# Kernel tuning notes

Measured on AMD Instinct MI355X. Metric: run time of the kernel, lower is better.

The kernel has to match this reference:

```python
import jax, jax.numpy as jnp
import numpy as np

H = 12  # num_heads (init kwarg)


def setup_inputs() -> dict:
    key = jax.random.key(0)
    ks = jax.random.split(key, 9)
    B, S, D, M = 2, 1025, 768, 4
    hw = S - 1
    x = jax.random.normal(ks[0], (B, S, D), dtype=jnp.float32)
    masks = jax.random.randint(ks[1], (B, M, hw), 0, 2, dtype=jnp.int32)
    init = lambda k: jax.random.normal(k, (D, D), dtype=jnp.float32) * 0.02
    return {
        'x': x, 'masks': masks,
        'Wq': init(ks[2]), 'bq': jnp.zeros((D,), jnp.float32),
        'Wk': init(ks[3]), 'bk': jnp.zeros((D,), jnp.float32),
        'Wv': init(ks[4]), 'bv': jnp.zeros((D,), jnp.float32),
    }


def reference(x, masks, Wq, bq, Wk, bk, Wv, bv):
    B, S, D = x.shape
    hd = D // H
    scale = 1.0 / jnp.sqrt(jnp.asarray(hd, x.dtype))

    def heads(t):  # (B,S,D) -> (B,H,S,hd)
        return t.reshape(B, S, H, hd).transpose(0, 2, 1, 3)

    q = heads(x @ Wq.T + bq)
    k = heads(x @ Wk.T + bk)
    v = heads(x @ Wv.T + bv)

    scores_ori = jnp.einsum('bhqd,bhkd->bhqk', q, k) * scale  # (B,H,S,S)
    attn = jax.nn.softmax(scores_ori, axis=-1)  # dropout is identity at eval
    h = jnp.einsum('bhqk,bhkd->bhqd', attn, v)
    h = h.transpose(0, 2, 1, 3).reshape(B, S, D)

    # ---- mask-expanded attention (torch.no_grad branch) ----
    Mk, hw = masks.shape[1], masks.shape[2]
    m = masks.astype(x.dtype)  # (B,M,hw)
    # pad: position 0 (CLS) gets 0, positions 1..hw get the mask
    new_masks = jnp.pad(m, ((0, 0), (0, 0), (1, S - 1 - hw)))  # (B,M,S)
    bias = -10000.0 * (1.0 - new_masks)  # additive mask bias
    new_scores = scores_ori[:, None] + bias[:, :, None, None, :]  # (B,M,H,S,S)
    new_attn = jax.nn.softmax(new_scores, axis=-1)
    new_h = jnp.einsum('bmhqk,bhkd->bmhqd', new_attn, v)  # v repeated per mask
    new_h = new_h.transpose(0, 1, 3, 2, 4).reshape(B * Mk, S, D)

    img_idx = jnp.repeat(jnp.arange(B), Mk)  # [0]*M + [1]*M + ...
    new_x = jnp.broadcast_to(x[:, None], (B, Mk, S, D)).reshape(B * Mk, S, D)
    return (h, new_h, img_idx, new_x)
```

## Files before the change

kernel.cpp:

```cpp
#include <hip/hip_runtime.h>

typedef float f32x4 __attribute__((ext_vector_type(4)));
typedef short s16x8 __attribute__((ext_vector_type(8)));

constexpr int B  = 2;
constexpr int S  = 1025;
constexpr int D  = 768;
constexpr int H  = 12;
constexpr int NM = 4;
constexpr int ROWS = B * S;
constexpr int BSD  = B * S * D;
constexpr int SP   = 1088;
constexpr int OUT_NEWH_OFF = BSD;
constexpr int OUT_IDX_OFF  = BSD + NM * BSD;
constexpr int OUT_NEWX_OFF = OUT_IDX_OFF + B * NM;

__device__ __forceinline__ unsigned short f2bf(float f) {
    unsigned u = __builtin_bit_cast(unsigned, f);
    u += 0x7FFF + ((u >> 16) & 1);
    return (unsigned short)(u >> 16);
}

__global__ __launch_bounds__(256, 2) void qkv_mfma_kernel(
    const float* __restrict__ x,
    const float* __restrict__ Wq, const float* __restrict__ bq,
    const float* __restrict__ Wk, const float* __restrict__ bk,
    const float* __restrict__ Wv, const float* __restrict__ bv,
    unsigned short* __restrict__ Qb, unsigned short* __restrict__ Kb,
    unsigned short* __restrict__ Vt)
{
    __shared__ unsigned short Xs[64 * 64];
    __shared__ unsigned short Wl[64 * 64];

    const int t = threadIdx.x;
    const int row0 = blockIdx.x * 64;
    const int yy = blockIdx.y;
    const int mt = yy / 12;
    const int col0 = (yy % 12) * 64;
    const float* W    = (mt == 0) ? Wq : (mt == 1) ? Wk : Wv;
    const float* bias = (mt == 0) ? bq : (mt == 1) ? bk : bv;

    const int w = t >> 6, l = t & 63, lq = l & 15, grp = l >> 4;

    f32x4 acc[4] = {};

    for (int k0 = 0; k0 < D; k0 += 64) {
        __syncthreads();
        #pragma unroll
        for (int st = 0; st < 2; ++st) {
            const int cid = t + st * 256;
            const int r = cid >> 3, c = cid & 7;
            {
                const int row = row0 + r;
                s16x8 v = {};
                if (row < ROWS) {
                    const float* p = x + (size_t)row * D + k0 + c * 8;
                    #pragma unroll
                    for (int i = 0; i < 8; i++) v[i] = (short)f2bf(p[i]);
                }
                *(s16x8*)&Xs[r * 64 + ((c ^ (r & 7)) * 8)] = v;
            }
            {
                const float* p = W + (size_t)(col0 + r) * D + k0 + c * 8;
                s16x8 v;
                #pragma unroll
                for (int i = 0; i < 8; i++) v[i] = (short)f2bf(p[i]);
                *(s16x8*)&Wl[r * 64 + ((c ^ (r & 7)) * 8)] = v;
            }
        }
        __syncthreads();

        s16x8 a[2];
        const int xr = w * 16 + lq;
        #pragma unroll
        for (int kh = 0; kh < 2; ++kh)
            a[kh] = *(const s16x8*)&Xs[xr * 64 + (((kh * 4 + grp) ^ (lq & 7)) * 8)];
        #pragma unroll
        for (int nt = 0; nt < 4; ++nt) {
            const int wr = nt * 16 + lq;
            #pragma unroll
            for (int kh = 0; kh < 2; ++kh) {
                s16x8 bfr = *(const s16x8*)&Wl[wr * 64 + (((kh * 4 + grp) ^ (lq & 7)) * 8)];
                acc[nt] = __builtin_amdgcn_mfma_f32_16x16x32_bf16(a[kh], bfr, acc[nt], 0, 0, 0);
            }
        }
    }

    #pragma unroll
    for (int nt = 0; nt < 4; ++nt) {
        const int col = col0 + nt * 16 + lq;
        const float bv_ = bias[col];
        #pragma unroll
        for (int r = 0; r < 4; ++r) {
            const int row = row0 + w * 16 + grp * 4 + r;
            if (row >= ROWS) continue;
            const unsigned short val = f2bf(acc[nt][r] + bv_);
            if (mt == 0)      Qb[(size_t)row * D + col] = val;
            else if (mt == 1) Kb[(size_t)row * D + col] = val;
            else {
                const int bb = (row >= S) ? 1 : 0;
                const int s  = row - bb * S;
                const int hh = col >> 6, dd = col & 63;
                Vt[((size_t)((bb * H + hh) * 64 + dd)) * SP + s] = val;
            }
        }
    }
}

__global__ void vt_pad_kernel(unsigned short* __restrict__ Vt)
{
    const int NPADC = SP - S;
    const int NPAD = B * H * 64 * NPADC;
    const int i = blockIdx.x * 256 + threadIdx.x;
    if (i < NPAD) {
        const int row = i / NPADC;
        const int s = S + (i % NPADC);
        Vt[(size_t)row * SP + s] = 0;
    }
}

__global__ __launch_bounds__(256, 2) void attn_mfma_kernel(
    const unsigned short* __restrict__ Qb, const unsigned short* __restrict__ Kb,
    const unsigned short* __restrict__ Vt, const int* __restrict__ masks,
    float* __restrict__ out_h, float* __restrict__ out_newh)
{
    __shared__ unsigned short Kl[64 * 64];
    __shared__ unsigned short Vl[64 * 64];
    __shared__ unsigned short Pl[4 * 16 * 64];
    __shared__ float          Mf[4][64];
    __shared__ unsigned short Mm[4 * 64];

    const int t = threadIdx.x;
    const int qt = blockIdx.x, hh = blockIdx.y, b = blockIdx.z;
    const int q0 = qt * 64;
    const int w = t >> 6, l = t & 63, lq = l & 15, grp = l >> 4;

    s16x8 qf[2] = {};
    {
        const int row = q0 + w * 16 + lq;
        if (row < S) {
            const unsigned short* p = Qb + (size_t)(b * S + row) * D + hh * 64 + grp * 8;
            qf[0] = *(const s16x8*)(p);
            qf[1] = *(const s16x8*)(p + 32);
        }
    }

    f32x4 acc[5][4] = {};
    float sums[5][4] = {};

    const int NT = 17;
    for (int it = 0; it < NT; ++it) {
        const int k0 = it * 64;
        __syncthreads();
        #pragma unroll
        for (int st = 0; st < 2; ++st) {
            const int cid = t + st * 256;
            const int r = cid >> 3, c = cid & 7;
            {
                const int p = k0 + r;
                uint4 v = make_uint4(0, 0, 0, 0);
                if (p < S) v = *(const uint4*)(Kb + (size_t)(b * S + p) * D + hh * 64 + c * 8);
                *(uint4*)&Kl[r * 64 + ((c ^ (r & 7)) * 8)] = v;
            }
            {
                uint4 v = *(const uint4*)(Vt + ((size_t)((b * H + hh) * 64 + r)) * SP + k0 + c * 8);
                *(uint4*)&Vl[r * 64 + ((c ^ (r & 7)) * 8)] = v;
            }
        }
        if (t < 64) {
            const int p = k0 + t;
            #pragma unroll
            for (int v = 0; v < 4; ++v) {
                const int m = (p >= 1 && p < S) ? masks[(size_t)(b * NM + v) * (S - 1) + p - 1] : 0;
                Mf[v][t] = (float)m;
                Mm[v * 64 + t] = m ? 0xFFFFu : 0u;
            }
        }
        __syncthreads();

        f32x4 qk[4] = {};
        #pragma unroll
        for (int kt = 0; kt < 4; ++kt) {
            const int kr = kt * 16 + lq;
            #pragma unroll
            for (int kh = 0; kh < 2; ++kh) {
                s16x8 kf = *(const s16x8*)&Kl[kr * 64 + (((kh * 4 + grp) ^ (lq & 7)) * 8)];
                qk[kt] = __builtin_amdgcn_mfma_f32_16x16x32_bf16(qf[kh], kf, qk[kt], 0, 0, 0);
            }
        }
        #pragma unroll
        for (int kt = 0; kt < 4; ++kt) {
            const int kloc = kt * 16 + lq;
            const int kg = k0 + kloc;
            const float mf0 = Mf[0][kloc], mf1 = Mf[1][kloc];
            const float mf2 = Mf[2][kloc], mf3 = Mf[3][kloc];
            #pragma unroll
            for (int r = 0; r < 4; ++r) {
                const float e = (kg < S) ? __expf(qk[kt][r] * 0.125f) : 0.f;
                sums[0][r] += e;
                sums[1][r] += mf0 * e; sums[2][r] += mf1 * e;
                sums[3][r] += mf2 * e; sums[4][r] += mf3 * e;
                const int q = grp * 4 + r;
                Pl[w * 1024 + q * 64 + (((kloc >> 3) ^ (q & 7)) * 8) + (kloc & 7)] = f2bf(e);
            }
        }
        __syncthreads();

        s16x8 pa[5][2];
        #pragma unroll
        for (int h2 = 0; h2 < 2; ++h2) {
            s16x8 ea = *(const s16x8*)&Pl[w * 1024 + lq * 64 + (((h2 * 4 + grp) ^ (lq & 7)) * 8)];
            pa[0][h2] = ea;
            #pragma unroll
            for (int v = 1; v < 5; ++v) {
                s16x8 mm = *(const s16x8*)&Mm[(v - 1) * 64 + (h2 * 4 + grp) * 8];
                pa[v][h2] = ea & mm;
            }
        }
        #pragma unroll
        for (int dt = 0; dt < 4; ++dt) {
            const int dr = dt * 16 + lq;
            #pragma unroll
            for (int h2 = 0; h2 < 2; ++h2) {
                s16x8 vb = *(const s16x8*)&Vl[dr * 64 + (((h2 * 4 + grp) ^ (lq & 7)) * 8)];
                #pragma unroll
                for (int v = 0; v < 5; ++v)
                    acc[v][dt] = __builtin_amdgcn_mfma_f32_16x16x32_bf16(pa[v][h2], vb, acc[v][dt], 0, 0, 0);
            }
        }
    }

    #pragma unroll
    for (int m = 1; m < 16; m <<= 1)
        #pragma unroll
        for (int v = 0; v < 5; ++v)
            #pragma unroll
            for (int r = 0; r < 4; ++r)
                sums[v][r] += __shfl_xor(sums[v][r], m);

    #pragma unroll
    for (int r = 0; r < 4; ++r) {
        const int q = q0 + w * 16 + grp * 4 + r;
        if (q >= S) continue;
        #pragma unroll
        for (int v = 0; v < 5; ++v) {
            const float inv = 1.0f / sums[v][r];
            float* outp = (v == 0)
                ? out_h    + (size_t)(b * S + q) * D + hh * 64 + lq
                : out_newh + (size_t)((b * NM + v - 1) * S + q) * D + hh * 64 + lq;
            #pragma unroll
            for (int dt = 0; dt < 4; ++dt)
                outp[dt * 16] = acc[v][dt][r] * inv;
        }
    }
}

__global__ __launch_bounds__(256) void tail_kernel(
    const float* __restrict__ x, float* __restrict__ out_newx,
    float* __restrict__ out_idx)
{
    const int SLAB4  = S * D / 4;
    const int TOTAL4 = B * NM * SLAB4;
    const float4* x4 = (const float4*)x;
    float4* o4 = (float4*)out_newx;
    for (int f = blockIdx.x * blockDim.x + threadIdx.x; f < TOTAL4;
         f += gridDim.x * blockDim.x) {
        const int bm  = f / SLAB4;
        const int rem = f - bm * SLAB4;
        o4[f] = x4[(bm >> 2) * SLAB4 + rem];
    }
    const int idx = blockIdx.x * blockDim.x + threadIdx.x;
    if (idx < B * NM) out_idx[idx] = (float)(idx >> 2);
}

extern "C" void kernel_launch(void* const* d_in, const int* in_sizes, int n_in,
                              void* d_out, int out_size, void* d_ws, size_t ws_size,
                              hipStream_t stream)
{
    const float* x     = (const float*)d_in[0];
    const int*   masks = (const int*)  d_in[1];
    const float* Wq    = (const float*)d_in[2];
    const float* bq    = (const float*)d_in[3];
    const float* Wk    = (const float*)d_in[4];
    const float* bk    = (const float*)d_in[5];
    const float* Wv    = (const float*)d_in[6];
    const float* bv    = (const float*)d_in[7];

    float* out = (float*)d_out;
    float* out_h    = out;
    float* out_newh = out + OUT_NEWH_OFF;
    float* out_idx  = out + OUT_IDX_OFF;
    float* out_newx = out + OUT_NEWX_OFF;

    unsigned short* Qb = (unsigned short*)d_ws;
    unsigned short* Kb = Qb + BSD;
    unsigned short* Vt = Kb + BSD;

    vt_pad_kernel<<<378, 256, 0, stream>>>(Vt);
    {
        dim3 grid(33, 36);
        qkv_mfma_kernel<<<grid, 256, 0, stream>>>(x, Wq, bq, Wk, bk, Wv, bv,
                                                  Qb, Kb, Vt);
    }
    {
        dim3 grid(17, H, B);
        attn_mfma_kernel<<<grid, 256, 0, stream>>>(Qb, Kb, Vt, masks,
                                                   out_h, out_newh);
    }
    tail_kernel<<<2048, 256, 0, stream>>>(x, out_newx, out_idx);
}
```

Baseline: 100.3 us.

## Pre-convert inputs to bf16 and double-buffer GEMM and attention with async LDS loads

A new conversion kernel casts x and the three weight matrices to bf16 once, using the output buffer as scratch, and also absorbs the Vt padding work. Both the QKV GEMM and the attention kernel now stage tiles with global_load_lds into double-buffered shared memory, so the next tile loads while the current one computes, and one barrier per iteration is removed. The attention kernel is reworked to 128 threads and 32 query rows per block, doubling the grid, with the P·V loop reordered to keep fewer registers live. In exchange it adds an extra pass over x and the weights, and it depends on the tail kernel overwriting the scratch region afterward.

```diff
diff --git a/kernel.cpp b/kernel.cpp
--- a/kernel.cpp
+++ b/kernel.cpp
@@ -6,6 +6,7 @@
 constexpr int B  = 2;
 constexpr int S  = 1025;
 constexpr int D  = 768;
+constexpr int DD = D * D;
 constexpr int H  = 12;
 constexpr int NM = 4;
 constexpr int ROWS = B * S;
@@ -21,66 +22,102 @@
     return (unsigned short)(u >> 16);
 }
 
+__device__ __forceinline__ void gll16(const void* g, void* l) {
+    __builtin_amdgcn_global_load_lds(
+        (const __attribute__((address_space(1))) void*)g,
+        (__attribute__((address_space(3))) void*)l, 16, 0, 0);
+}
+
+__global__ __launch_bounds__(256) void conv_kernel(
+    const float* __restrict__ x, const float* __restrict__ Wq,
+    const float* __restrict__ Wk, const float* __restrict__ Wv,
+    unsigned short* __restrict__ xb, unsigned short* __restrict__ Wb,
+    unsigned short* __restrict__ Vt)
+{
+    constexpr int NX8 = BSD / 8;
+    constexpr int NW8 = DD / 8;
+    constexpr int TOT = NX8 + 3 * NW8;
+    const int tid = blockIdx.x * 256 + threadIdx.x;
+    for (int c = tid; c < TOT; c += gridDim.x * 256) {
+        const float* src;
+        unsigned short* dst;
+        if (c < NX8) { src = x + (size_t)c * 8; dst = xb + (size_t)c * 8; }
+        else {
+            const int cc = c - NX8;
+            const int mt = cc / NW8;
+            const int rr = cc - mt * NW8;
+            src = ((mt == 0) ? Wq : (mt == 1) ? Wk : Wv) + (size_t)rr * 8;
+            dst = Wb + (size_t)mt * DD + (size_t)rr * 8;
+        }
+        const float4 a = *(const float4*)src;
+        const float4 b2 = *(const float4*)(src + 4);
+        s16x8 v;
+        v[0] = (short)f2bf(a.x);  v[1] = (short)f2bf(a.y);
+        v[2] = (short)f2bf(a.z);  v[3] = (short)f2bf(a.w);
+        v[4] = (short)f2bf(b2.x); v[5] = (short)f2bf(b2.y);
+        v[6] = (short)f2bf(b2.z); v[7] = (short)f2bf(b2.w);
+        *(s16x8*)dst = v;
+    }
+    constexpr int NPADC = SP - S;
+    constexpr int NPAD = B * H * 64 * NPADC;
+    if (tid < NPAD) {
+        const int row = tid / NPADC;
+        const int s = S + (tid % NPADC);
+        Vt[(size_t)row * SP + s] = 0;
+    }
+}
+
 __global__ __launch_bounds__(256, 2) void qkv_mfma_kernel(
-    const float* __restrict__ x,
-    const float* __restrict__ Wq, const float* __restrict__ bq,
-    const float* __restrict__ Wk, const float* __restrict__ bk,
-    const float* __restrict__ Wv, const float* __restrict__ bv,
+    const unsigned short* __restrict__ xb, const unsigned short* __restrict__ Wb,
+    const float* __restrict__ bq, const float* __restrict__ bk,
+    const float* __restrict__ bv,
     unsigned short* __restrict__ Qb, unsigned short* __restrict__ Kb,
     unsigned short* __restrict__ Vt)
 {
-    __shared__ unsigned short Xs[64 * 64];
-    __shared__ unsigned short Wl[64 * 64];
+    __shared__ __align__(16) unsigned short Xs[2][64 * 64];
+    __shared__ __align__(16) unsigned short Wl[2][64 * 64];
 
     const int t = threadIdx.x;
     const int row0 = blockIdx.x * 64;
     const int yy = blockIdx.y;
     const int mt = yy / 12;
     const int col0 = (yy % 12) * 64;
-    const float* W    = (mt == 0) ? Wq : (mt == 1) ? Wk : Wv;
     const float* bias = (mt == 0) ? bq : (mt == 1) ? bk : bv;
+    const unsigned short* Wsrc = Wb + (size_t)mt * DD;
 
     const int w = t >> 6, l = t & 63, lq = l & 15, grp = l >> 4;
 
+    auto stage = [&](int buf, int k0) {
+        #pragma unroll
+        for (int i = 0; i < 2; ++i) {
+            const int slot = i * 256 + t;
+            const int r = slot >> 3, cl = slot & 7;
+            const int cg = cl ^ (r & 7);
+            int row = row0 + r; if (row > ROWS - 1) row = ROWS - 1;
+            gll16(xb + (size_t)row * D + k0 + cg * 8, &Xs[buf][slot * 8]);
+            gll16(Wsrc + (size_t)(col0 + r) * D + k0 + cg * 8, &Wl[buf][slot * 8]);
+        }
+    };
+
     f32x4 acc[4] = {};
-
-    for (int k0 = 0; k0 < D; k0 += 64) {
+    stage(0, 0);
+
+    for (int ks = 0; ks < 12; ++ks) {
+        const int cur = ks & 1;
         __syncthreads();
-        #pragma unroll
-        for (int st = 0; st < 2; ++st) {
-            const int cid = t + st * 256;
-            const int r = cid >> 3, c = cid & 7;
-            {
-                const int row = row0 + r;
-                s16x8 v = {};
-                if (row < ROWS) {
-                    const float* p = x + (size_t)row * D + k0 + c * 8;
-                    #pragma unroll
-                    for (int i = 0; i < 8; i++) v[i] = (short)f2bf(p[i]);
-                }
-                *(s16x8*)&Xs[r * 64 + ((c ^ (r & 7)) * 8)] = v;
-            }
-            {
-                const float* p = W + (size_t)(col0 + r) * D + k0 + c * 8;
-                s16x8 v;
-                #pragma unroll
-                for (int i = 0; i < 8; i++) v[i] = (short)f2bf(p[i]);
-                *(s16x8*)&Wl[r * 64 + ((c ^ (r & 7)) * 8)] = v;
-            }
-        }
-        __syncthreads();
+        if (ks + 1 < 12) stage(cur ^ 1, (ks + 1) * 64);
 
         s16x8 a[2];
         const int xr = w * 16 + lq;
         #pragma unroll
         for (int kh = 0; kh < 2; ++kh)
-            a[kh] = *(const s16x8*)&Xs[xr * 64 + (((kh * 4 + grp) ^ (lq & 7)) * 8)];
+            a[kh] = *(const s16x8*)&Xs[cur][xr * 64 + (((kh * 4 + grp) ^ (xr & 7)) * 8)];
         #pragma unroll
         for (int nt = 0; nt < 4; ++nt) {
             const int wr = nt * 16 + lq;
             #pragma unroll
             for (int kh = 0; kh < 2; ++kh) {
-                s16x8 bfr = *(const s16x8*)&Wl[wr * 64 + (((kh * 4 + grp) ^ (lq & 7)) * 8)];
+                s16x8 bfr = *(const s16x8*)&Wl[cur][wr * 64 + (((kh * 4 + grp) ^ (wr & 7)) * 8)];
                 acc[nt] = __builtin_amdgcn_mfma_f32_16x16x32_bf16(a[kh], bfr, acc[nt], 0, 0, 0);
             }
         }
@@ -107,32 +144,20 @@
     }
 }
 
-__global__ void vt_pad_kernel(unsigned short* __restrict__ Vt)
-{
-    const int NPADC = SP - S;
-    const int NPAD = B * H * 64 * NPADC;
-    const int i = blockIdx.x * 256 + threadIdx.x;
-    if (i < NPAD) {
-        const int row = i / NPADC;
-        const int s = S + (i % NPADC);
-        Vt[(size_t)row * SP + s] = 0;
-    }
-}
-
-__global__ __launch_bounds__(256, 2) void attn_mfma_kernel(
+__global__ __launch_bounds__(128, 2) void attn_mfma_kernel(
     const unsigned short* __restrict__ Qb, const unsigned short* __restrict__ Kb,
     const unsigned short* __restrict__ Vt, const int* __restrict__ masks,
     float* __restrict__ out_h, float* __restrict__ out_newh)
 {
-    __shared__ unsigned short Kl[64 * 64];
-    __shared__ unsigned short Vl[64 * 64];
-    __shared__ unsigned short Pl[4 * 16 * 64];
-    __shared__ float          Mf[4][64];
-    __shared__ unsigned short Mm[4 * 64];
+    __shared__ __align__(16) unsigned short Kl[2][64 * 64];
+    __shared__ __align__(16) unsigned short Vl[2][64 * 64];
+    __shared__ __align__(16) unsigned short Pl[2][16 * 64];
+    __shared__ __align__(16) float          Mf[2][4][64];
+    __shared__ __align__(16) unsigned short Mm[2][4 * 64];
 
     const int t = threadIdx.x;
     const int qt = blockIdx.x, hh = blockIdx.y, b = blockIdx.z;
-    const int q0 = qt * 64;
+    const int q0 = qt * 32;
     const int w = t >> 6, l = t & 63, lq = l & 15, grp = l >> 4;
 
     s16x8 qf[2] = {};
@@ -145,38 +170,48 @@
         }
     }
 
+    const unsigned short* Kbase = Kb + (size_t)b * S * D + hh * 64;
+    const unsigned short* Vbase = Vt + (size_t)(b * H + hh) * 64 * SP;
+
+    auto stage = [&](int buf, int it) {
+        const int k0 = it * 64;
+        #pragma unroll
+        for (int i = 0; i < 4; ++i) {
+            const int slot = i * 128 + t;
+            const int r = slot >> 3, cl = slot & 7;
+            const int cg = cl ^ (r & 7);
+            int p = k0 + r; if (p > S - 1) p = S - 1;
+            gll16(Kbase + (size_t)p * D + cg * 8, &Kl[buf][slot * 8]);
+        }
+        #pragma unroll
+        for (int i = 0; i < 4; ++i) {
+            const int slot = i * 128 + t;
+            const int r = slot >> 3, cl = slot & 7;
+            const int cg = cl ^ (r & 7);
+            gll16(Vbase + (size_t)r * SP + k0 + cg * 8, &Vl[buf][slot * 8]);
+        }
+        #pragma unroll
+        for (int j = 0; j < 2; ++j) {
+            const int idx = j * 128 + t;
+            const int v = idx >> 6, kk = idx & 63;
+            const int p = k0 + kk;
+            const int m = (p >= 1 && p < S) ? masks[(size_t)(b * NM + v) * (S - 1) + p - 1] : 0;
+            Mf[buf][v][kk] = (float)m;
+            Mm[buf][v * 64 + kk] = m ? 0xFFFFu : 0u;
+        }
+    };
+
     f32x4 acc[5][4] = {};
     float sums[5][4] = {};
 
-    const int NT = 17;
+    stage(0, 0);
+
+    constexpr int NT = 17;
     for (int it = 0; it < NT; ++it) {
+        const int cur = it & 1;
+        __syncthreads();
+        if (it + 1 < NT) stage(cur ^ 1, it + 1);
         const int k0 = it * 64;
-        __syncthreads();
-        #pragma unroll
-        for (int st = 0; st < 2; ++st) {
-            const int cid = t + st * 256;
-            const int r = cid >> 3, c = cid & 7;
-            {
-                const int p = k0 + r;
-                uint4 v = make_uint4(0, 0, 0, 0);
-                if (p < S) v = *(const uint4*)(Kb + (size_t)(b * S + p) * D + hh * 64 + c * 8);
-                *(uint4*)&Kl[r * 64 + ((c ^ (r & 7)) * 8)] = v;
-            }
-            {
-                uint4 v = *(const uint4*)(Vt + ((size_t)((b * H + hh) * 64 + r)) * SP + k0 + c * 8);
-                *(uint4*)&Vl[r * 64 + ((c ^ (r & 7)) * 8)] = v;
-            }
-        }
-        if (t < 64) {
-            const int p = k0 + t;
-            #pragma unroll
-            for (int v = 0; v < 4; ++v) {
-                const int m = (p >= 1 && p < S) ? masks[(size_t)(b * NM + v) * (S - 1) + p - 1] : 0;
-                Mf[v][t] = (float)m;
-                Mm[v * 64 + t] = m ? 0xFFFFu : 0u;
-            }
-        }
-        __syncthreads();
 
         f32x4 qk[4] = {};
         #pragma unroll
@@ -184,16 +219,17 @@
             const int kr = kt * 16 + lq;
             #pragma unroll
             for (int kh = 0; kh < 2; ++kh) {
-                s16x8 kf = *(const s16x8*)&Kl[kr * 64 + (((kh * 4 + grp) ^ (lq & 7)) * 8)];
+                s16x8 kf = *(const s16x8*)&Kl[cur][kr * 64 + (((kh * 4 + grp) ^ (kr & 7)) * 8)];
                 qk[kt] = __builtin_amdgcn_mfma_f32_16x16x32_bf16(qf[kh], kf, qk[kt], 0, 0, 0);
             }
         }
+
         #pragma unroll
         for (int kt = 0; kt < 4; ++kt) {
             const int kloc = kt * 16 + lq;
             const int kg = k0 + kloc;
-            const float mf0 = Mf[0][kloc], mf1 = Mf[1][kloc];
-            const float mf2 = Mf[2][kloc], mf3 = Mf[3][kloc];
+            const float mf0 = Mf[cur][0][kloc], mf1 = Mf[cur][1][kloc];
+            const float mf2 = Mf[cur][2][kloc], mf3 = Mf[cur][3][kloc];
             #pragma unroll
             for (int r = 0; r < 4; ++r) {
                 const float e = (kg < S) ? __expf(qk[kt][r] * 0.125f) : 0.f;
@@ -201,31 +237,27 @@
                 sums[1][r] += mf0 * e; sums[2][r] += mf1 * e;
                 sums[3][r] += mf2 * e; sums[4][r] += mf3 * e;
                 const int q = grp * 4 + r;
-                Pl[w * 1024 + q * 64 + (((kloc >> 3) ^ (q & 7)) * 8) + (kloc & 7)] = f2bf(e);
-            }
-        }
-        __syncthreads();
-
-        s16x8 pa[5][2];
+                Pl[w][q * 64 + (((kloc >> 3) ^ (q & 7)) * 8) + (kloc & 7)] = f2bf(e);
+            }
+        }
+
         #pragma unroll
         for (int h2 = 0; h2 < 2; ++h2) {
-            s16x8 ea = *(const s16x8*)&Pl[w * 1024 + lq * 64 + (((h2 * 4 + grp) ^ (lq & 7)) * 8)];
-            pa[0][h2] = ea;
+            s16x8 ea = *(const s16x8*)&Pl[w][lq * 64 + (((h2 * 4 + grp) ^ (lq & 7)) * 8)];
+            s16x8 pa[5];
+            pa[0] = ea;
             #pragma unroll
             for (int v = 1; v < 5; ++v) {
-                s16x8 mm = *(const s16x8*)&Mm[(v - 1) * 64 + (h2 * 4 + grp) * 8];
-                pa[v][h2] = ea & mm;
-            }
-        }
-        #pragma unroll
-        for (int dt = 0; dt < 4; ++dt) {
-            const int dr = dt * 16 + lq;
-            #pragma unroll
-            for (int h2 = 0; h2 < 2; ++h2) {
-                s16x8 vb = *(const s16x8*)&Vl[dr * 64 + (((h2 * 4 + grp) ^ (lq & 7)) * 8)];
+                s16x8 mm = *(const s16x8*)&Mm[cur][(v - 1) * 64 + (h2 * 4 + grp) * 8];
+                pa[v] = ea & mm;
+            }
+            #pragma unroll
+            for (int dt = 0; dt < 4; ++dt) {
+                const int dr = dt * 16 + lq;
+                s16x8 vb = *(const s16x8*)&Vl[cur][dr * 64 + (((h2 * 4 + grp) ^ (dr & 7)) * 8)];
                 #pragma unroll
                 for (int v = 0; v < 5; ++v)
-                    acc[v][dt] = __builtin_amdgcn_mfma_f32_16x16x32_bf16(pa[v][h2], vb, acc[v][dt], 0, 0, 0);
+                    acc[v][dt] = __builtin_amdgcn_mfma_f32_16x16x32_bf16(pa[v], vb, acc[v][dt], 0, 0, 0);
             }
         }
     }
@@ -296,15 +328,17 @@
     unsigned short* Kb = Qb + BSD;
     unsigned short* Vt = Kb + BSD;
 
-    vt_pad_kernel<<<378, 256, 0, stream>>>(Vt);
+    unsigned short* xb = (unsigned short*)out_newx;
+    unsigned short* Wb = xb + BSD;
+
+    conv_kernel<<<1634, 256, 0, stream>>>(x, Wq, Wk, Wv, xb, Wb, Vt);
     {
         dim3 grid(33, 36);
-        qkv_mfma_kernel<<<grid, 256, 0, stream>>>(x, Wq, bq, Wk, bk, Wv, bv,
-                                                  Qb, Kb, Vt);
+        qkv_mfma_kernel<<<grid, 256, 0, stream>>>(xb, Wb, bq, bk, bv, Qb, Kb, Vt);
     }
     {
-        dim3 grid(17, H, B);
-        attn_mfma_kernel<<<grid, 256, 0, stream>>>(Qb, Kb, Vt, masks,
+        dim3 grid(33, H, B);
+        attn_mfma_kernel<<<grid, 128, 0, stream>>>(Qb, Kb, Vt, masks,
                                                    out_h, out_newh);
     }
     tail_kernel<<<2048, 256, 0, stream>>>(x, out_newx, out_idx);
```

Result: no change. 99.97 us (-0.4%).
